# Optimization experiments

Measured on AMD Instinct MI355X. Metric: run time of the kernel, lower is better.

The kernel has to match this reference:

```python
import jax, jax.numpy as jnp
import numpy as np

# PGA G(3,0,1): 16 blades, bitmask index order: e0->bit0, e1->bit1, e2->bit2, e3->bit3
N = 16
PSS = 15  # index of pseudoscalar e0123


def _sign(a, b):
    # canonical reordering sign for merging sorted blades a, b (bitmasks)
    s = 0
    a >>= 1
    while a:
        s += bin(a & b).count("1")
        a >>= 1
    return -1.0 if (s & 1) else 1.0


def _build_tables():
    GP = np.zeros((N, N, N), dtype=np.float32)  # geometric product table
    WE = np.zeros((N, N, N), dtype=np.float32)  # wedge (outer) product table
    for a in range(N):
        for b in range(N):
            s = _sign(a, b)
            if (a & b) == 0:
                WE[a, b, a | b] = s
            if not (a & b & 1):  # degenerate metric: e0^2 = 0 kills shared-e0 terms
                GP[a, b, a ^ b] = s
    # right-complement dual: e_A ^ dual(e_A) = e0123 (metric-free Poincare dual)
    D = np.zeros((N, N), dtype=np.float32)
    for a in range(N):
        c = PSS ^ a
        D[c, a] = _sign(a, c)
    UD = np.linalg.inv(D).astype(np.float32)  # undual (signed permutation inverse)
    # 9 Pin(3,0,1)-equivariant linear basis maps: grade projections P0..P4 and
    # left-multiplication by e0 composed with P0..P3
    g = np.array([bin(i).count("1") for i in range(N)])
    B = np.zeros((9, N, N), dtype=np.float32)
    for k in range(5):
        B[k] = np.diag((g == k).astype(np.float32))
    for k in range(4):
        for i in range(N):
            if g[i] == k and not (i & 1):
                B[5 + k, i | 1, i] = 1.0  # e0 * e_A, e0 prepends in canonical order: sign +1
    return GP, WE, D, UD, B

_GP, _WE, _D, _UD, _B = _build_tables()


def _equi_linear(x, w, b):
    # x: [..., in, 16], w: [out, in, 9], b: [out] (bias on scalar blade only)
    out = jnp.einsum("oib,bjk,...ik->...oj", w, jnp.asarray(_B), x)
    return out.at[..., 0].add(b)


def _geometric_product(x, y):
    return jnp.einsum("...i,...j,ijk->...k", x, y, jnp.asarray(_GP))


def _equi_join(x, y, ref):
    D = jnp.asarray(_D)
    xd = jnp.einsum("ji,...i->...j", D, x)
    yd = jnp.einsum("ji,...i->...j", D, y)
    j = jnp.einsum("...i,...j,ijk->...k", xd, yd, jnp.asarray(_WE))
    j = jnp.einsum("ji,...i->...j", jnp.asarray(_UD), j)
    return ref[..., PSS:PSS + 1] * j  # scale by reference pseudoscalar coefficient


def setup_inputs() -> dict:
    key = jax.random.key(0)
    k = jax.random.split(key, 6)
    B_, S, CIN, COUT, H = 4, 4096, 64, 64, 128
    x = jax.random.normal(k[0], (B_, S, CIN, N), dtype=jnp.float32)
    ref = jax.random.normal(k[1], (B_, S, 1, N), dtype=jnp.float32)
    w_bilinear = jax.random.normal(k[2], (2 * H, CIN, 9), dtype=jnp.float32) / np.sqrt(CIN * 3)
    b_bilinear = jax.random.normal(k[3], (2 * H,), dtype=jnp.float32) * 0.01
    w_next = jax.random.normal(k[4], (COUT, H, 9), dtype=jnp.float32) / np.sqrt(H * 3)
    b_next = jax.random.normal(k[5], (COUT,), dtype=jnp.float32) * 0.01
    return {"x": x, "ref": ref, "w_bilinear": w_bilinear, "b_bilinear": b_bilinear,
            "w_next": w_next, "b_next": b_next}


def reference(x, ref, w_bilinear, b_bilinear, w_next, b_next):
    h = _equi_linear(x, w_bilinear, b_bilinear)            # [B,S,2*hidden,16]
    l_geo, r_geo, l_join, r_join = jnp.split(h, 4, axis=-2)  # each [B,S,hidden//2,16]
    out = jnp.concatenate(
        [_geometric_product(l_geo, r_geo), _equi_join(l_join, r_join, ref)], axis=-2
    )                                                       # [B,S,hidden,16]
    return _equi_linear(out, w_next, b_next)                # [B,S,out,16]
```

## Files before the change

kernel.cpp:

```cpp
#include <hip/hip_runtime.h>


namespace {

constexpr int popc4(int v){int c=0;while(v){c+=v&1;v>>=1;}return c;}
constexpr float sgnf(int a,int b){int s=0;a>>=1;while(a){s+=popc4(a&b);a>>=1;}return (s&1)?-1.f:1.f;}

struct Tabs { float gp[16][16]; float jn[16][16]; };
constexpr Tabs mk(){
    Tabs t{};
    for(int a=0;a<16;a++)for(int b=0;b<16;b++){
        t.gp[a][b] = (a&b&1) ? 0.f : sgnf(a,b);
        if((a|b)==15){
            const int k = a&b;
            t.jn[a][b] = sgnf(a,15^a)*sgnf(b,15^b)*sgnf(15^a,15^b)*sgnf(k,15^k);
        } else t.jn[a][b] = 0.f;
    }
    return t;
}
constexpr Tabs TB = mk();
constexpr int GE[8] = {0,1,1,2,1,2,2,3};

constexpr int OFF1(int j){ return (j>>1)*49152 + ((j&1)?16384:0); }
constexpr int OFF2(int j){ return (j>>1)*24576 + ((j&1)?8192:0);  }
constexpr int W1B_ELEMS = 393216;
constexpr int W2B_ELEMS = 196608;

typedef short bf16x8 __attribute__((ext_vector_type(8)));
typedef float f32x4  __attribute__((ext_vector_type(4)));

__device__ inline unsigned short f2bf(float f){
    unsigned int u = __float_as_uint(f);
    u = u + 0x7fffu + ((u >> 16) & 1u);
    return (unsigned short)(u >> 16);
}
__device__ inline unsigned pack2(float a, float b){
    return (unsigned)f2bf(a) | ((unsigned)f2bf(b) << 16);
}

}

__global__ void prep_w(const float* __restrict__ w1, const float* __restrict__ w2,
                       unsigned short* __restrict__ w1b, unsigned short* __restrict__ w2b)
{
    int idx = blockIdx.x * 256 + threadIdx.x;
    if (idx < W1B_ELEMS) {
        const int p = idx / 49152, rem = idx - p*49152;
        float v;
        if (rem < 16384) {
            const int j = 2*p, o = rem >> 6, k = rem & 63;
            v = w1[(o*64 + k)*9 + __popc(j)];
        } else {
            const int j = 2*p + 1, r2 = rem - 16384, o = r2 >> 7, k = r2 & 127;
            const int g = __popc(j), i = k & 63, r = (k < 64) ? g + 4 : g;
            v = w1[(o*64 + i)*9 + r];
        }
        w1b[idx] = f2bf(v);
    } else {
        idx -= W1B_ELEMS;
        if (idx < W2B_ELEMS) {
            const int p = idx / 24576, rem = idx - p*24576;
            float v;
            if (rem < 8192) {
                const int j = 2*p, o = rem >> 7, k = rem & 127;
                v = w2[(o*128 + k)*9 + __popc(j)];
            } else {
                const int j = 2*p + 1, r2 = rem - 8192, o = r2 >> 8, k = r2 & 255;
                const int g = __popc(j), i = k & 127, r = (k < 128) ? g + 4 : g;
                v = w2[(o*128 + i)*9 + r];
            }
            w2b[idx] = f2bf(v);
        }
    }
}

__global__ __launch_bounds__(512, 2) void gb_mfma(
    const float* __restrict__ x, const float* __restrict__ ref,
    const float* __restrict__ b1, const float* __restrict__ b2,
    const unsigned short* __restrict__ w1b, const unsigned short* __restrict__ w2b,
    float* __restrict__ out)
{
    __shared__ __attribute__((aligned(16))) char X1[32768];
    __shared__ __attribute__((aligned(16))) char X2[65536];
    __shared__ float lref[16];

    const int t   = threadIdx.x;
    const int bid = blockIdx.x;
    const int w   = t >> 6;
    const int l   = t & 63;
    const int ln  = l & 15;
    const int lh  = l >> 4;
    const int swz = (ln & 7) << 4;
    const int p0  = bid * 16;

    const int st  = w >> 2;
    const int grp = w & 3;
    const int f0  = (st == 0) ? grp : grp + 8;
    const int oA  = f0*16 + ln;
    const int oB  = (f0+4)*16 + ln;

    {
        const int spos = t >> 5;
        const int si0  = (t & 31) * 2;
        const float* gsrc = x + ((long)(p0 + spos))*1024 + si0*16;
        float4 v[8];
        #pragma unroll
        for (int a = 0; a < 8; ++a) v[a] = *(const float4*)(gsrc + a*4);
        const int ws_ = (spos & 7) << 4;
        #pragma unroll
        for (int b = 0; b < 16; ++b) {
            const int e = b >> 1, s = b & 1;
            const float va = ((const float*)&v[b>>2])[b&3];
            const float vb = ((const float*)&v[4 + (b>>2)])[b&3];
            *(unsigned*)(X1 + ((((e*16 + spos) << 8) + (s << 7) + (si0 << 1)) ^ ws_)) = pack2(va, vb);
        }
        if (t < 16) lref[t] = ref[((long)(p0 + t))*16 + 15];
    }
    __syncthreads();

    f32x4 left[16];
    #pragma unroll
    for (int j = 0; j < 16; ++j) left[j] = (f32x4)0.f;

    bf16x8 pa[4][4];
    #pragma unroll
    for (int jp = 0; jp < 4; ++jp) {
        const int Kj = (jp & 1) ? 128 : 64;
        const unsigned short* Aj = w1b + OFF1(jp);
        #pragma unroll
        for (int kf = 0; kf < ((jp & 1) ? 4 : 2); ++kf)
            pa[jp][kf] = *(const bf16x8*)(Aj + oA*Kj + kf*32 + lh*8);
    }
    #pragma unroll
    for (int j = 0; j < 16; ++j) {
        const int e = j >> 1, nkf = (j & 1) ? 4 : 2;
        bf16x8 cur[4];
        #pragma unroll
        for (int kf = 0; kf < nkf; ++kf) cur[kf] = pa[j & 3][kf];
        if (j < 12) {
            const int jn = j + 4, Kn = (jn & 1) ? 128 : 64;
            const unsigned short* An = w1b + OFF1(jn);
            #pragma unroll
            for (int kf = 0; kf < ((jn & 1) ? 4 : 2); ++kf)
                pa[j & 3][kf] = *(const bf16x8*)(An + oA*Kn + kf*32 + lh*8);
        }
        #pragma unroll
        for (int kf = 0; kf < nkf; ++kf) {
            const bf16x8 bx = *(const bf16x8*)(X1 + ((((e*16 + ln) << 8) + ((kf*32 + lh*8) << 1)) ^ swz));
            left[j] = __builtin_amdgcn_mfma_f32_16x16x32_bf16(cur[kf], bx, left[j], 0, 0, 0);
        }
    }
    #pragma unroll
    for (int r = 0; r < 4; ++r) left[0][r] += b1[f0*16 + lh*4 + r];

    f32x4 prod[16];
    #pragma unroll
    for (int j = 0; j < 16; ++j) prod[j] = (f32x4)0.f;

    bf16x8 pb[2][4];
    #pragma unroll
    for (int jp = 0; jp < 2; ++jp) {
        const int Kj = (jp & 1) ? 128 : 64;
        const unsigned short* Aj = w1b + OFF1(jp);
        #pragma unroll
        for (int kf = 0; kf < ((jp & 1) ? 4 : 2); ++kf)
            pb[jp][kf] = *(const bf16x8*)(Aj + oB*Kj + kf*32 + lh*8);
    }
    #pragma unroll
    for (int j = 0; j < 16; ++j) {
        const int e = j >> 1, nkf = (j & 1) ? 4 : 2;
        bf16x8 cur[4];
        #pragma unroll
        for (int kf = 0; kf < nkf; ++kf) cur[kf] = pb[j & 1][kf];
        if (j < 14) {
            const int jn = j + 2, Kn = (jn & 1) ? 128 : 64;
            const unsigned short* An = w1b + OFF1(jn);
            #pragma unroll
            for (int kf = 0; kf < ((jn & 1) ? 4 : 2); ++kf)
                pb[j & 1][kf] = *(const bf16x8*)(An + oB*Kn + kf*32 + lh*8);
        }
        f32x4 right = (f32x4)0.f;
        #pragma unroll
        for (int kf = 0; kf < nkf; ++kf) {
            const bf16x8 bx = *(const bf16x8*)(X1 + ((((e*16 + ln) << 8) + ((kf*32 + lh*8) << 1)) ^ swz));
            right = __builtin_amdgcn_mfma_f32_16x16x32_bf16(cur[kf], bx, right, 0, 0, 0);
        }
        if (j == 0) {
            #pragma unroll
            for (int r = 0; r < 4; ++r) right[r] += b1[(f0+4)*16 + lh*4 + r];
        }
        if (st == 0) {
            #pragma unroll
            for (int A = 0; A < 16; ++A) {
                constexpr auto& G = TB.gp;
                if (G[A][0] || true) {}
                if (TB.gp[A][0] == TB.gp[A][0]) {}
            }
            #pragma unroll
            for (int A = 0; A < 16; ++A) {
                if (TB.gp[A][j] > 0.f)      prod[A ^ j] += left[A] * right;
                else if (TB.gp[A][j] < 0.f) prod[A ^ j] -= left[A] * right;
            }
        } else {
            #pragma unroll
            for (int A = 0; A < 16; ++A) {
                if (TB.jn[A][j] > 0.f)      prod[A & j] += left[A] * right;
                else if (TB.jn[A][j] < 0.f) prod[A & j] -= left[A] * right;
            }
        }
    }
    if (st == 1) {
        const float rv = lref[ln];
        #pragma unroll
        for (int j = 0; j < 16; ++j) prod[j] *= rv;
    }

    {
        const int pc0 = st*64 + grp*16;
        #pragma unroll
        for (int e2 = 0; e2 < 8; ++e2)
            #pragma unroll
            for (int s = 0; s < 2; ++s)
                #pragma unroll
                for (int rp = 0; rp < 4; rp += 2) {
                    const int cc = pc0 + lh*4 + rp;
                    *(unsigned*)(X2 + ((((e2*16 + ln) << 9) + (s << 8) + (cc << 1)) ^ swz)) =
                        pack2(prod[2*e2 + s][rp], prod[2*e2 + s][rp + 1]);
                }
    }
    __syncthreads();

    const int o2base = grp * 16;
    f32x4 acc2[8];
    #pragma unroll
    for (int jj = 0; jj < 8; ++jj) acc2[jj] = (f32x4)0.f;

    bf16x8 pc[2][8];
    {
        const int j2 = st*8, K2 = (j2 & 1) ? 256 : 128;
        const unsigned short* A2 = w2b + OFF2(j2);
        #pragma unroll
        for (int kf = 0; kf < ((j2 & 1) ? 8 : 4); ++kf)
            pc[0][kf] = *(const bf16x8*)(A2 + (o2base + ln)*K2 + kf*32 + lh*8);
    }
    #pragma unroll
    for (int jj = 0; jj < 8; ++jj) {
        const int j2 = st*8 + jj, e2 = j2 >> 1, nkf = (j2 & 1) ? 8 : 4;
        bf16x8 cur[8];
        #pragma unroll
        for (int kf = 0; kf < nkf; ++kf) cur[kf] = pc[jj & 1][kf];
        if (jj < 7) {
            const int jn = st*8 + jj + 1, Kn = (jn & 1) ? 256 : 128;
            const unsigned short* An = w2b + OFF2(jn);
            #pragma unroll
            for (int kf = 0; kf < ((jn & 1) ? 8 : 4); ++kf)
                pc[(jj + 1) & 1][kf] = *(const bf16x8*)(An + (o2base + ln)*Kn + kf*32 + lh*8);
        }
        #pragma unroll
        for (int kf = 0; kf < nkf; ++kf) {
            const bf16x8 bx = *(const bf16x8*)(X2 + ((((e2*16 + ln) << 9) + ((kf*32 + lh*8) << 1)) ^ swz));
            acc2[jj] = __builtin_amdgcn_mfma_f32_16x16x32_bf16(cur[kf], bx, acc2[jj], 0, 0, 0);
        }
    }
    if (st == 0) {
        #pragma unroll
        for (int r = 0; r < 4; ++r) acc2[0][r] += b2[o2base + lh*4 + r];
    }
    __syncthreads();

    {
        #pragma unroll
        for (int r = 0; r < 4; ++r) {
            const int o2 = o2base + lh*4 + r;
            const int raw0 = (ln << 12) + (o2 << 6) + (st << 5);
            *(float4*)(X2 + (raw0 ^ swz)) =
                make_float4(acc2[0][r], acc2[1][r], acc2[2][r], acc2[3][r]);
            *(float4*)(X2 + ((raw0 + 16) ^ swz)) =
                make_float4(acc2[4][r], acc2[5][r], acc2[6][r], acc2[7][r]);
        }
    }
    __syncthreads();
    {
        #pragma unroll
        for (int it = 0; it < 8; ++it) {
            const int idx = it*512 + t;
            const int pos = idx >> 8, off = idx & 255;
            const float4 vv = *(const float4*)(X2 + (((pos << 12) + (off << 4)) ^ ((pos & 7) << 4)));
            *(float4*)(out + ((long)(p0 + pos))*1024 + off*4) = vv;
        }
    }
}

__global__ __launch_bounds__(256, 1) void gb_fused_f32(
    const float* __restrict__ x, const float* __restrict__ ref,
    const float* __restrict__ w1, const float* __restrict__ b1,
    const float* __restrict__ w2, const float* __restrict__ b2,
    float* __restrict__ out)
{
    __shared__ float lds[16384];
    __shared__ float lrefs[8];
    const int t = threadIdx.x;
    const int p0 = blockIdx.x * 8;
    {
        const float4* xg = reinterpret_cast<const float4*>(x) + (size_t)p0 * 256;
        float4* xl = reinterpret_cast<float4*>(lds);
        #pragma unroll
        for (int r = 0; r < 8; ++r) xl[r*256 + t] = xg[r*256 + t];
        if (t < 8) lrefs[t] = ref[(p0 + t)*16 + 15];
    }
    __syncthreads();
    const int c    = t & 127;
    const int half = t >> 7;
    const int ca   = (c < 64) ? c : (c + 64);
    const int cb   = ca + 64;
    float acc[4][2][16];
    #pragma unroll
    for (int q = 0; q < 4; ++q)
        #pragma unroll
        for (int s = 0; s < 2; ++s)
            #pragma unroll
            for (int j = 0; j < 16; ++j) acc[q][s][j] = 0.f;
    for (int i = 0; i < 64; ++i) {
        float wa[9], wb[9];
        #pragma unroll
        for (int r = 0; r < 9; ++r) { wa[r] = w1[(ca*64+i)*9 + r]; wb[r] = w1[(cb*64+i)*9 + r]; }
        #pragma unroll
        for (int q = 0; q < 4; ++q) {
            const float* xv = lds + (half*4 + q)*1024 + i*16;
            float xr[16];
            #pragma unroll
            for (int j4 = 0; j4 < 4; ++j4) {
                const float4 v = *reinterpret_cast<const float4*>(xv + 4*j4);
                xr[4*j4+0]=v.x; xr[4*j4+1]=v.y; xr[4*j4+2]=v.z; xr[4*j4+3]=v.w;
            }
            #pragma unroll
            for (int e = 0; e < 8; ++e) {
                const int ge = GE[e];
                const float xe = xr[2*e], xo = xr[2*e+1];
                acc[q][0][2*e]   += wa[ge]   * xe;
                acc[q][0][2*e+1] += wa[ge+1] * xo;
                acc[q][0][2*e+1] += wa[ge+5] * xe;
                acc[q][1][2*e]   += wb[ge]   * xe;
                acc[q][1][2*e+1] += wb[ge+1] * xo;
                acc[q][1][2*e+1] += wb[ge+5] * xe;
            }
        }
    }
    {
        const float ba = b1[ca], bb = b1[cb];
        #pragma unroll
        for (int q = 0; q < 4; ++q) { acc[q][0][0] += ba; acc[q][1][0] += bb; }
    }
    __syncthreads();
    #pragma unroll
    for (int q = 0; q < 4; ++q) {
        float prod[16];
        #pragma unroll
        for (int j = 0; j < 16; ++j) prod[j] = 0.f;
        if (c < 64) {
            #pragma unroll
            for (int A = 0; A < 16; ++A)
                #pragma unroll
                for (int B = 0; B < 16; ++B)
                    if (TB.gp[A][B] != 0.f)
                        prod[A ^ B] += TB.gp[A][B] * acc[q][0][A] * acc[q][1][B];
        } else {
            #pragma unroll
            for (int A = 0; A < 16; ++A)
                #pragma unroll
                for (int B = 0; B < 16; ++B)
                    if (TB.jn[A][B] != 0.f)
                        prod[A & B] += TB.jn[A][B] * acc[q][0][A] * acc[q][1][B];
            const float rp = lrefs[half*4 + q];
            #pragma unroll
            for (int j = 0; j < 16; ++j) prod[j] *= rp;
        }
        const int pos = half*4 + q;
        #pragma unroll
        for (int j4 = 0; j4 < 4; ++j4)
            *reinterpret_cast<float4*>(&lds[(pos*4 + j4)*512 + c*4]) =
                make_float4(prod[4*j4], prod[4*j4+1], prod[4*j4+2], prod[4*j4+3]);
    }
    __syncthreads();
    const int o    = t & 63;
    const int slot = t >> 6;
    float oacc[2][16];
    #pragma unroll
    for (int e2 = 0; e2 < 2; ++e2)
        #pragma unroll
        for (int j = 0; j < 16; ++j) oacc[e2][j] = 0.f;
    for (int i = 0; i < 128; ++i) {
        float wv[9];
        #pragma unroll
        for (int r = 0; r < 9; ++r) wv[r] = w2[(o*128+i)*9 + r];
        #pragma unroll
        for (int e2 = 0; e2 < 2; ++e2) {
            const int pos = slot*2 + e2;
            float xr[16];
            #pragma unroll
            for (int j4 = 0; j4 < 4; ++j4) {
                const float4 v = *reinterpret_cast<const float4*>(&lds[(pos*4 + j4)*512 + i*4]);
                xr[4*j4+0]=v.x; xr[4*j4+1]=v.y; xr[4*j4+2]=v.z; xr[4*j4+3]=v.w;
            }
            #pragma unroll
            for (int e = 0; e < 8; ++e) {
                const int ge = GE[e];
                oacc[e2][2*e]   += wv[ge]   * xr[2*e];
                oacc[e2][2*e+1] += wv[ge+1] * xr[2*e+1];
                oacc[e2][2*e+1] += wv[ge+5] * xr[2*e];
            }
        }
    }
    {
        const float bo = b2[o];
        #pragma unroll
        for (int e2 = 0; e2 < 2; ++e2) {
            oacc[e2][0] += bo;
            const int pos = p0 + slot*2 + e2;
            float* og = out + (size_t)pos*1024 + o*16;
            #pragma unroll
            for (int j4 = 0; j4 < 4; ++j4)
                *reinterpret_cast<float4*>(og + 4*j4) =
                    make_float4(oacc[e2][4*j4], oacc[e2][4*j4+1],
                                oacc[e2][4*j4+2], oacc[e2][4*j4+3]);
        }
    }
}

extern "C" void kernel_launch(void* const* d_in, const int* in_sizes, int n_in,
                              void* d_out, int out_size, void* d_ws, size_t ws_size,
                              hipStream_t stream)
{
    const float* x  = (const float*)d_in[0];
    const float* rf = (const float*)d_in[1];
    const float* w1 = (const float*)d_in[2];
    const float* b1 = (const float*)d_in[3];
    const float* w2 = (const float*)d_in[4];
    const float* b2 = (const float*)d_in[5];
    float* out = (float*)d_out;

    const size_t need = (size_t)(W1B_ELEMS + W2B_ELEMS) * sizeof(unsigned short);
    if (ws_size >= need) {
        unsigned short* w1b = (unsigned short*)d_ws;
        unsigned short* w2b = w1b + W1B_ELEMS;
        prep_w<<<(W1B_ELEMS + W2B_ELEMS)/256, 256, 0, stream>>>(w1, w2, w1b, w2b);
        gb_mfma<<<1024, 512, 0, stream>>>(x, rf, b1, b2, w1b, w2b, out);
    } else {
        gb_fused_f32<<<2048, 256, 0, stream>>>(x, rf, w1, b1, w2, b2, out);
    }
}
```

Baseline: 162.8 us.

## Store bf16 weights row-contiguous per output and pad LDS strides instead of XOR swizzle

Reorganizes the prepared bf16 weight buffers so each output row holds all blade/grade K-slices contiguously, letting each lane walk one pointer with constant offsets. The register double-buffered weight prefetch is removed, and weights are loaded right before each MFMA. LDS tiles switch from XOR swizzling to padded row strides, which simplifies address math in staging, the GEMMs and the epilogue. The risk is exposed global-load latency without explicit prefetch, and larger LDS footprint that could affect occupancy.

```diff
diff --git a/kernel.cpp b/kernel.cpp
--- a/kernel.cpp
+++ b/kernel.cpp
@@ -21,10 +21,16 @@
 constexpr Tabs TB = mk();
 constexpr int GE[8] = {0,1,1,2,1,2,2,3};
 
-constexpr int OFF1(int j){ return (j>>1)*49152 + ((j&1)?16384:0); }
-constexpr int OFF2(int j){ return (j>>1)*24576 + ((j&1)?8192:0);  }
-constexpr int W1B_ELEMS = 393216;
-constexpr int W2B_ELEMS = 196608;
+constexpr int BASE1(int j){ return (j>>1)*192 + ((j&1)?64:0); }
+constexpr int BASE2(int j){ return (j>>1)*384 + ((j&1)?128:0); }
+constexpr int W1C_ELEMS = 256*1536;
+constexpr int W2C_ELEMS = 64*3072;
+
+constexpr int X1_STRIDE = 272;
+constexpr int X2_STRIDE = 544;
+constexpr int EP_STRIDE = 4112;
+constexpr int X1_BYTES  = 128*X1_STRIDE;
+constexpr int X2_BYTES  = 128*X2_STRIDE;
 
 typedef short bf16x8 __attribute__((ext_vector_type(8)));
 typedef float f32x4  __attribute__((ext_vector_type(4)));
@@ -41,35 +47,35 @@
 }
 
 __global__ void prep_w(const float* __restrict__ w1, const float* __restrict__ w2,
-                       unsigned short* __restrict__ w1b, unsigned short* __restrict__ w2b)
+                       unsigned short* __restrict__ w1c, unsigned short* __restrict__ w2c)
 {
     int idx = blockIdx.x * 256 + threadIdx.x;
-    if (idx < W1B_ELEMS) {
-        const int p = idx / 49152, rem = idx - p*49152;
+    if (idx < W1C_ELEMS) {
+        const int o = idx / 1536, r = idx - o*1536;
+        const int p = r / 192, q = r - p*192;
         float v;
-        if (rem < 16384) {
-            const int j = 2*p, o = rem >> 6, k = rem & 63;
-            v = w1[(o*64 + k)*9 + __popc(j)];
+        if (q < 64) {
+            v = w1[(o*64 + q)*9 + popc4(2*p)];
         } else {
-            const int j = 2*p + 1, r2 = rem - 16384, o = r2 >> 7, k = r2 & 127;
-            const int g = __popc(j), i = k & 63, r = (k < 64) ? g + 4 : g;
-            v = w1[(o*64 + i)*9 + r];
-        }
-        w1b[idx] = f2bf(v);
+            const int j = 2*p + 1, k = q - 64, g = popc4(j);
+            v = (k < 64) ? w1[(o*64 + k)*9 + g + 4]
+                         : w1[(o*64 + (k - 64))*9 + g];
+        }
+        w1c[idx] = f2bf(v);
     } else {
-        idx -= W1B_ELEMS;
-        if (idx < W2B_ELEMS) {
-            const int p = idx / 24576, rem = idx - p*24576;
+        idx -= W1C_ELEMS;
+        if (idx < W2C_ELEMS) {
+            const int o = idx / 3072, r = idx - o*3072;
+            const int p = r / 384, q = r - p*384;
             float v;
-            if (rem < 8192) {
-                const int j = 2*p, o = rem >> 7, k = rem & 127;
-                v = w2[(o*128 + k)*9 + __popc(j)];
+            if (q < 128) {
+                v = w2[(o*128 + q)*9 + popc4(2*p)];
             } else {
-                const int j = 2*p + 1, r2 = rem - 8192, o = r2 >> 8, k = r2 & 255;
-                const int g = __popc(j), i = k & 127, r = (k < 128) ? g + 4 : g;
-                v = w2[(o*128 + i)*9 + r];
-            }
-            w2b[idx] = f2bf(v);
+                const int j = 2*p + 1, k = q - 128, g = popc4(j);
+                v = (k < 128) ? w2[(o*128 + k)*9 + g + 4]
+                              : w2[(o*128 + (k - 128))*9 + g];
+            }
+            w2c[idx] = f2bf(v);
         }
     }
 }
@@ -77,11 +83,11 @@
 __global__ __launch_bounds__(512, 2) void gb_mfma(
     const float* __restrict__ x, const float* __restrict__ ref,
     const float* __restrict__ b1, const float* __restrict__ b2,
-    const unsigned short* __restrict__ w1b, const unsigned short* __restrict__ w2b,
+    const unsigned short* __restrict__ w1c, const unsigned short* __restrict__ w2c,
     float* __restrict__ out)
 {
-    __shared__ __attribute__((aligned(16))) char X1[32768];
-    __shared__ __attribute__((aligned(16))) char X2[65536];
+    __shared__ __attribute__((aligned(16))) char X1[X1_BYTES];
+    __shared__ __attribute__((aligned(16))) char X2[X2_BYTES];
     __shared__ float lref[16];
 
     const int t   = threadIdx.x;
@@ -90,14 +96,19 @@
     const int l   = t & 63;
     const int ln  = l & 15;
     const int lh  = l >> 4;
-    const int swz = (ln & 7) << 4;
     const int p0  = bid * 16;
 
     const int st  = w >> 2;
     const int grp = w & 3;
     const int f0  = (st == 0) ? grp : grp + 8;
-    const int oA  = f0*16 + ln;
-    const int oB  = (f0+4)*16 + ln;
+
+    const unsigned short* pA = w1c + (f0*16 + ln)*1536;
+    const unsigned short* pB = w1c + ((f0+4)*16 + ln)*1536;
+    const unsigned short* pC = w2c + (grp*16 + ln)*3072 + 1536;
+    const int vX1 = ln*X1_STRIDE + lh*16;
+    const int vX2 = ln*X2_STRIDE + lh*16;
+    const int vX2w = ln*X2_STRIDE + w*32 + lh*8;
+    const int vEp  = ln*EP_STRIDE + grp*1024 + lh*256 + st*32;
 
     {
         const int spos = t >> 5;
@@ -106,13 +117,13 @@
         float4 v[8];
         #pragma unroll
         for (int a = 0; a < 8; ++a) v[a] = *(const float4*)(gsrc + a*4);
-        const int ws_ = (spos & 7) << 4;
+        char* base = X1 + spos*X1_STRIDE + si0*2;
         #pragma unroll
         for (int b = 0; b < 16; ++b) {
             const int e = b >> 1, s = b & 1;
             const float va = ((const float*)&v[b>>2])[b&3];
             const float vb = ((const float*)&v[4 + (b>>2)])[b&3];
-            *(unsigned*)(X1 + ((((e*16 + spos) << 8) + (s << 7) + (si0 << 1)) ^ ws_)) = pack2(va, vb);
+            *(unsigned*)(base + e*16*X1_STRIDE + s*128) = pack2(va, vb);
         }
         if (t < 16) lref[t] = ref[((long)(p0 + t))*16 + 15];
     }
@@ -122,32 +133,14 @@
     #pragma unroll
     for (int j = 0; j < 16; ++j) left[j] = (f32x4)0.f;
 
-    bf16x8 pa[4][4];
-    #pragma unroll
-    for (int jp = 0; jp < 4; ++jp) {
-        const int Kj = (jp & 1) ? 128 : 64;
-        const unsigned short* Aj = w1b + OFF1(jp);
-        #pragma unroll
-        for (int kf = 0; kf < ((jp & 1) ? 4 : 2); ++kf)
-            pa[jp][kf] = *(const bf16x8*)(Aj + oA*Kj + kf*32 + lh*8);
-    }
     #pragma unroll
     for (int j = 0; j < 16; ++j) {
         const int e = j >> 1, nkf = (j & 1) ? 4 : 2;
-        bf16x8 cur[4];
-        #pragma unroll
-        for (int kf = 0; kf < nkf; ++kf) cur[kf] = pa[j & 3][kf];
-        if (j < 12) {
-            const int jn = j + 4, Kn = (jn & 1) ? 128 : 64;
-            const unsigned short* An = w1b + OFF1(jn);
-            #pragma unroll
-            for (int kf = 0; kf < ((jn & 1) ? 4 : 2); ++kf)
-                pa[j & 3][kf] = *(const bf16x8*)(An + oA*Kn + kf*32 + lh*8);
-        }
         #pragma unroll
         for (int kf = 0; kf < nkf; ++kf) {
-            const bf16x8 bx = *(const bf16x8*)(X1 + ((((e*16 + ln) << 8) + ((kf*32 + lh*8) << 1)) ^ swz));
-            left[j] = __builtin_amdgcn_mfma_f32_16x16x32_bf16(cur[kf], bx, left[j], 0, 0, 0);
+            const bf16x8 a  = *(const bf16x8*)(pA + BASE1(j) + kf*32 + lh*8);
+            const bf16x8 bx = *(const bf16x8*)(X1 + vX1 + e*16*X1_STRIDE + kf*64);
+            left[j] = __builtin_amdgcn_mfma_f32_16x16x32_bf16(a, bx, left[j], 0, 0, 0);
         }
     }
     #pragma unroll
@@ -157,45 +150,21 @@
     #pragma unroll
     for (int j = 0; j < 16; ++j) prod[j] = (f32x4)0.f;
 
-    bf16x8 pb[2][4];
-    #pragma unroll
-    for (int jp = 0; jp < 2; ++jp) {
-        const int Kj = (jp & 1) ? 128 : 64;
-        const unsigned short* Aj = w1b + OFF1(jp);
-        #pragma unroll
-        for (int kf = 0; kf < ((jp & 1) ? 4 : 2); ++kf)
-            pb[jp][kf] = *(const bf16x8*)(Aj + oB*Kj + kf*32 + lh*8);
-    }
     #pragma unroll
     for (int j = 0; j < 16; ++j) {
         const int e = j >> 1, nkf = (j & 1) ? 4 : 2;
-        bf16x8 cur[4];
-        #pragma unroll
-        for (int kf = 0; kf < nkf; ++kf) cur[kf] = pb[j & 1][kf];
-        if (j < 14) {
-            const int jn = j + 2, Kn = (jn & 1) ? 128 : 64;
-            const unsigned short* An = w1b + OFF1(jn);
-            #pragma unroll
-            for (int kf = 0; kf < ((jn & 1) ? 4 : 2); ++kf)
-                pb[j & 1][kf] = *(const bf16x8*)(An + oB*Kn + kf*32 + lh*8);
-        }
         f32x4 right = (f32x4)0.f;
         #pragma unroll
         for (int kf = 0; kf < nkf; ++kf) {
-            const bf16x8 bx = *(const bf16x8*)(X1 + ((((e*16 + ln) << 8) + ((kf*32 + lh*8) << 1)) ^ swz));
-            right = __builtin_amdgcn_mfma_f32_16x16x32_bf16(cur[kf], bx, right, 0, 0, 0);
+            const bf16x8 a  = *(const bf16x8*)(pB + BASE1(j) + kf*32 + lh*8);
+            const bf16x8 bx = *(const bf16x8*)(X1 + vX1 + e*16*X1_STRIDE + kf*64);
+            right = __builtin_amdgcn_mfma_f32_16x16x32_bf16(a, bx, right, 0, 0, 0);
         }
         if (j == 0) {
             #pragma unroll
             for (int r = 0; r < 4; ++r) right[r] += b1[(f0+4)*16 + lh*4 + r];
         }
         if (st == 0) {
-            #pragma unroll
-            for (int A = 0; A < 16; ++A) {
-                constexpr auto& G = TB.gp;
-                if (G[A][0] || true) {}
-                if (TB.gp[A][0] == TB.gp[A][0]) {}
-            }
             #pragma unroll
             for (int A = 0; A < 16; ++A) {
                 if (TB.gp[A][j] > 0.f)      prod[A ^ j] += left[A] * right;
@@ -215,79 +184,51 @@
         for (int j = 0; j < 16; ++j) prod[j] *= rv;
     }
 
-    {
-        const int pc0 = st*64 + grp*16;
-        #pragma unroll
-        for (int e2 = 0; e2 < 8; ++e2)
-            #pragma unroll
-            for (int s = 0; s < 2; ++s)
-                #pragma unroll
-                for (int rp = 0; rp < 4; rp += 2) {
-                    const int cc = pc0 + lh*4 + rp;
-                    *(unsigned*)(X2 + ((((e2*16 + ln) << 9) + (s << 8) + (cc << 1)) ^ swz)) =
-                        pack2(prod[2*e2 + s][rp], prod[2*e2 + s][rp + 1]);
-                }
-    }
-    __syncthreads();
-
-    const int o2base = grp * 16;
+    #pragma unroll
+    for (int e2 = 0; e2 < 8; ++e2)
+        #pragma unroll
+        for (int s = 0; s < 2; ++s)
+            #pragma unroll
+            for (int rp = 0; rp < 4; rp += 2)
+                *(unsigned*)(X2 + vX2w + e2*16*X2_STRIDE + s*256 + rp*2) =
+                    pack2(prod[2*e2 + s][rp], prod[2*e2 + s][rp + 1]);
+    __syncthreads();
+
     f32x4 acc2[8];
     #pragma unroll
     for (int jj = 0; jj < 8; ++jj) acc2[jj] = (f32x4)0.f;
 
-    bf16x8 pc[2][8];
-    {
-        const int j2 = st*8, K2 = (j2 & 1) ? 256 : 128;
-        const unsigned short* A2 = w2b + OFF2(j2);
-        #pragma unroll
-        for (int kf = 0; kf < ((j2 & 1) ? 8 : 4); ++kf)
-            pc[0][kf] = *(const bf16x8*)(A2 + (o2base + ln)*K2 + kf*32 + lh*8);
-    }
     #pragma unroll
     for (int jj = 0; jj < 8; ++jj) {
-        const int j2 = st*8 + jj, e2 = j2 >> 1, nkf = (j2 & 1) ? 8 : 4;
-        bf16x8 cur[8];
-        #pragma unroll
-        for (int kf = 0; kf < nkf; ++kf) cur[kf] = pc[jj & 1][kf];
-        if (jj < 7) {
-            const int jn = st*8 + jj + 1, Kn = (jn & 1) ? 256 : 128;
-            const unsigned short* An = w2b + OFF2(jn);
-            #pragma unroll
-            for (int kf = 0; kf < ((jn & 1) ? 8 : 4); ++kf)
-                pc[(jj + 1) & 1][kf] = *(const bf16x8*)(An + (o2base + ln)*Kn + kf*32 + lh*8);
-        }
+        const int j2 = st*8 + jj;
+        const int e2 = j2 >> 1, nkf = (j2 & 1) ? 8 : 4;
         #pragma unroll
         for (int kf = 0; kf < nkf; ++kf) {
-            const bf16x8 bx = *(const bf16x8*)(X2 + ((((e2*16 + ln) << 9) + ((kf*32 + lh*8) << 1)) ^ swz));
-            acc2[jj] = __builtin_amdgcn_mfma_f32_16x16x32_bf16(cur[kf], bx, acc2[jj], 0, 0, 0);
+            const bf16x8 a  = *(const bf16x8*)(pC + (BASE2(j2) - 1536) + kf*32 + lh*8);
+            const bf16x8 bx = *(const bf16x8*)(X2 + vX2 + e2*16*X2_STRIDE + kf*64);
+            acc2[jj] = __builtin_amdgcn_mfma_f32_16x16x32_bf16(a, bx, acc2[jj], 0, 0, 0);
         }
     }
     if (st == 0) {
         #pragma unroll
-        for (int r = 0; r < 4; ++r) acc2[0][r] += b2[o2base + lh*4 + r];
-    }
-    __syncthreads();
-
-    {
-        #pragma unroll
-        for (int r = 0; r < 4; ++r) {
-            const int o2 = o2base + lh*4 + r;
-            const int raw0 = (ln << 12) + (o2 << 6) + (st << 5);
-            *(float4*)(X2 + (raw0 ^ swz)) =
-                make_float4(acc2[0][r], acc2[1][r], acc2[2][r], acc2[3][r]);
-            *(float4*)(X2 + ((raw0 + 16) ^ swz)) =
-                make_float4(acc2[4][r], acc2[5][r], acc2[6][r], acc2[7][r]);
-        }
-    }
-    __syncthreads();
-    {
-        #pragma unroll
-        for (int it = 0; it < 8; ++it) {
-            const int idx = it*512 + t;
-            const int pos = idx >> 8, off = idx & 255;
-            const float4 vv = *(const float4*)(X2 + (((pos << 12) + (off << 4)) ^ ((pos & 7) << 4)));
-            *(float4*)(out + ((long)(p0 + pos))*1024 + off*4) = vv;
-        }
+        for (int r = 0; r < 4; ++r) acc2[0][r] += b2[grp*16 + lh*4 + r];
+    }
+    __syncthreads();
+
+    #pragma unroll
+    for (int r = 0; r < 4; ++r) {
+        *(float4*)(X2 + vEp + r*64)      = make_float4(acc2[0][r], acc2[1][r], acc2[2][r], acc2[3][r]);
+        *(float4*)(X2 + vEp + r*64 + 16) = make_float4(acc2[4][r], acc2[5][r], acc2[6][r], acc2[7][r]);
+    }
+    __syncthreads();
+    {
+        const int pr = t >> 8;
+        const int off = t & 255;
+        const char* rbase = X2 + pr*EP_STRIDE + off*16;
+        float* gbase = out + ((long)(p0 + pr))*1024 + off*4;
+        #pragma unroll
+        for (int it = 0; it < 8; ++it)
+            *(float4*)(gbase + (long)it*2048) = *(const float4*)(rbase + it*2*EP_STRIDE);
     }
 }
 
@@ -439,12 +380,12 @@
     const float* b2 = (const float*)d_in[5];
     float* out = (float*)d_out;
 
-    const size_t need = (size_t)(W1B_ELEMS + W2B_ELEMS) * sizeof(unsigned short);
+    const size_t need = (size_t)(W1C_ELEMS + W2C_ELEMS) * sizeof(unsigned short);
     if (ws_size >= need) {
-        unsigned short* w1b = (unsigned short*)d_ws;
-        unsigned short* w2b = w1b + W1B_ELEMS;
-        prep_w<<<(W1B_ELEMS + W2B_ELEMS)/256, 256, 0, stream>>>(w1, w2, w1b, w2b);
-        gb_mfma<<<1024, 512, 0, stream>>>(x, rf, b1, b2, w1b, w2b, out);
+        unsigned short* w1c = (unsigned short*)d_ws;
+        unsigned short* w2c = w1c + W1C_ELEMS;
+        prep_w<<<(W1C_ELEMS + W2C_ELEMS)/256, 256, 0, stream>>>(w1, w2, w1c, w2c);
+        gb_mfma<<<1024, 512, 0, stream>>>(x, rf, b1, b2, w1c, w2c, out);
     } else {
         gb_fused_f32<<<2048, 256, 0, stream>>>(x, rf, w1, b1, w2, b2, out);
     }
```

Result: slower. 166.1 us (+2.0%).
